# Optimization experiments

Hardware: AMD Instinct MI355X
Metric: run time of the kernel (lower is better)

Reference implementation:

```python
import jax, jax.numpy as jnp
import numpy as np

C_S, C_P, C_H, H, P_QK, P_V = 384, 128, 16, 12, 4, 8
B, N = 1, 512
INF = 1e5
EPS = 1e-8


def quat_to_rot(q):
    w, x, y, z = q[..., 0], q[..., 1], q[..., 2], q[..., 3]
    return jnp.stack([
        jnp.stack([1 - 2 * (y * y + z * z), 2 * (x * y - w * z), 2 * (x * z + w * y)], -1),
        jnp.stack([2 * (x * y + w * z), 1 - 2 * (x * x + z * z), 2 * (y * z - w * x)], -1),
        jnp.stack([2 * (x * z - w * y), 2 * (y * z + w * x), 1 - 2 * (x * x + y * y)], -1),
    ], -2)


def layer_norm(x, g, b):
    m = x.mean(-1, keepdims=True)
    v = ((x - m) ** 2).mean(-1, keepdims=True)
    return (x - m) * jax.lax.rsqrt(v + 1e-5) * g + b


def setup_inputs():
    key = jax.random.key(0)
    ks = iter(jax.random.split(key, 64))

    def w(shape, scale=0.02):
        return jax.random.normal(next(ks), shape, dtype=jnp.float32) * scale

    inp = {}
    inp['s'] = jax.random.normal(next(ks), (B, N, C_S), dtype=jnp.float32)
    inp['p'] = jax.random.normal(next(ks), (B, N, N, C_P), dtype=jnp.float32)
    q = jax.random.normal(next(ks), (B, N, 4), dtype=jnp.float32)
    inp['rot'] = quat_to_rot(q / jnp.linalg.norm(q, axis=-1, keepdims=True))
    inp['trans'] = jax.random.normal(next(ks), (B, N, 3), dtype=jnp.float32)
    inp['mask'] = jnp.ones((B, N), dtype=jnp.float32)
    inp['w_q'] = w((C_S, H * C_H)); inp['b_q'] = jnp.zeros((H * C_H,), jnp.float32)
    inp['w_kv'] = w((C_S, 2 * H * C_H)); inp['b_kv'] = jnp.zeros((2 * H * C_H,), jnp.float32)
    inp['w_qp'] = w((C_S, H * P_QK * 3)); inp['b_qp'] = jnp.zeros((H * P_QK * 3,), jnp.float32)
    inp['w_kvp'] = w((C_S, H * (P_QK + P_V) * 3)); inp['b_kvp'] = jnp.zeros((H * (P_QK + P_V) * 3,), jnp.float32)
    inp['w_b'] = w((C_P, H)); inp['b_b'] = jnp.zeros((H,), jnp.float32)
    inp['head_w'] = w((H,), 0.5)
    d_out = H * (C_H + C_P + P_V * 4)  # 2112
    inp['w_o'] = w((d_out, C_S)); inp['b_o'] = jnp.zeros((C_S,), jnp.float32)
    inp['ln1_g'] = jnp.ones((C_S,), jnp.float32); inp['ln1_b'] = jnp.zeros((C_S,), jnp.float32)
    for i in (1, 2, 3):
        inp['tw%d' % i] = w((C_S, C_S)); inp['tb%d' % i] = jnp.zeros((C_S,), jnp.float32)
    inp['ln2_g'] = jnp.ones((C_S,), jnp.float32); inp['ln2_b'] = jnp.zeros((C_S,), jnp.float32)
    inp['bb_w'] = w((C_S, 6)); inp['bb_b'] = jnp.zeros((6,), jnp.float32)
    return inp


def forward(s, p, rot, trans, mask, w_q, b_q, w_kv, b_kv, w_qp, b_qp, w_kvp, b_kvp,
            w_b, b_b, head_w, w_o, b_o, ln1_g, ln1_b,
            tw1, tb1, tw2, tb2, tw3, tb3, ln2_g, ln2_b, bb_w, bb_b):
    # ---- Invariant Point Attention ----
    q = (s @ w_q + b_q).reshape(B, N, H, C_H)
    k, v = jnp.split((s @ w_kv + b_kv).reshape(B, N, H, 2 * C_H), 2, axis=-1)
    qp = (s @ w_qp + b_qp).reshape(B, N, H * P_QK, 3)
    qp = (jnp.einsum('bnij,bnpj->bnpi', rot, qp) + trans[:, :, None, :]).reshape(B, N, H, P_QK, 3)
    kvp = (s @ w_kvp + b_kvp).reshape(B, N, H * (P_QK + P_V), 3)
    kvp = (jnp.einsum('bnij,bnpj->bnpi', rot, kvp) + trans[:, :, None, :]).reshape(B, N, H, P_QK + P_V, 3)
    kp, vp = kvp[..., :P_QK, :], kvp[..., P_QK:, :]
    bias = p @ w_b + b_b  # [B,N,N,H]
    a = jnp.einsum('bihc,bjhc->bhij', q, k) * float(np.sqrt(1.0 / (3 * C_H)))
    a = a + float(np.sqrt(1.0 / 3)) * jnp.transpose(bias, (0, 3, 1, 2))
    d2 = ((qp[:, :, None] - kp[:, None]) ** 2).sum(-1)  # [B,N,N,H,Pqk]
    hw = jax.nn.softplus(head_w) * float(np.sqrt(1.0 / (3 * (P_QK * 9.0 / 2))))
    pt_att = -0.5 * (d2 * hw[:, None]).sum(-1)  # [B,N,N,H]
    sq_mask = (mask[:, :, None] * mask[:, None, :] - 1.0) * INF  # [B,N,N]
    a = jax.nn.softmax(a + jnp.transpose(pt_att, (0, 3, 1, 2)) + sq_mask[:, None], axis=-1)
    o = jnp.einsum('bhij,bjhc->bihc', a, v).reshape(B, N, H * C_H)
    op = jnp.einsum('bhij,bjhpc->bihpc', a, vp) - trans[:, :, None, None, :]
    op = jnp.einsum('bnji,bnhpj->bnhpi', rot, op)  # invert-apply frames
    op_norm = jnp.sqrt((op ** 2).sum(-1) + EPS)  # [B,N,H,Pv]
    o_pair = jnp.einsum('bhij,bijc->bihc', a, p).reshape(B, N, H * C_P)
    cat = jnp.concatenate([o, op.reshape(B, N, H * P_V * 3), op_norm.reshape(B, N, H * P_V), o_pair], -1)
    s = s + cat @ w_o + b_o
    s = layer_norm(s, ln1_g, ln1_b)
    # ---- structure transition (1 layer, residual + LN) ----
    h = jax.nn.relu(s @ tw1 + tb1)
    h = jax.nn.relu(h @ tw2 + tb2)
    s = layer_norm(s + h @ tw3 + tb3, ln2_g, ln2_b)
    # ---- backbone update + frame compose ----
    upd = s @ bb_w + bb_b  # [B,N,6]
    quat = jnp.concatenate([jnp.ones((B, N, 1), s.dtype), upd[..., :3]], -1)
    quat = quat / jnp.linalg.norm(quat, axis=-1, keepdims=True)
    r_u = quat_to_rot(quat)
    rot_new = jnp.einsum('bnij,bnjk->bnik', rot, r_u)
    trans_new = jnp.einsum('bnij,bnj->bni', rot, upd[..., 3:]) + trans
    return s, rot_new, trans_new


def reference(s, p, rot, trans, mask, w_q, b_q, w_kv, b_kv, w_qp, b_qp, w_kvp, b_kvp,
              w_b, b_b, head_w, w_o, b_o, ln1_g, ln1_b,
              tw1, tb1, tw2, tb2, tw3, tb3, ln2_g, ln2_b, bb_w, bb_b):
    return forward(s, p, rot, trans, mask, w_q, b_q, w_kv, b_kv, w_qp, b_qp, w_kvp, b_kvp,
                   w_b, b_b, head_w, w_o, b_o, ln1_g, ln1_b,
                   tw1, tb1, tw2, tb2, tw3, tb3, ln2_g, ln2_b, bb_w, bb_b)
```

## Files before the change

kernel.cpp:

```cpp
#include <hip/hip_runtime.h>
#include <math.h>

#define N 512
#define CS 384
#define CP 128
#define CH 16
#define NH 12
#define NN (N*N)
#define DCAT 2112
#define INFV 100000.0f

__device__ __constant__ float SC_QK = 0.14433756729740643f;
#define SC_B  0.57735026918962576f
#define HW_SC 0.13608276348795434f

typedef __attribute__((ext_vector_type(8))) short bf16x8;
typedef __attribute__((ext_vector_type(4))) float f32x4;
typedef __attribute__((ext_vector_type(4))) short sh4;
typedef unsigned short ushort_t;

__device__ inline short f2bf(float v) {
    unsigned u = __builtin_bit_cast(unsigned, v);
    u += 0x7FFF + ((u >> 16) & 1);
    return (short)(u >> 16);
}
__device__ inline float bf2f(ushort_t u) {
    unsigned x = ((unsigned)u) << 16;
    return __builtin_bit_cast(float, x);
}
__device__ __forceinline__ unsigned cvtpk(float a, float b) {
    unsigned r;
    asm("v_cvt_pk_bf16_f32 %0, %1, %2" : "=v"(r) : "v"(a), "v"(b));
    return r;
}

__device__ __forceinline__ void gload16(const void* g, void* l) {
    __builtin_amdgcn_global_load_lds(
        (const __attribute__((address_space(1))) unsigned int*)g,
        (__attribute__((address_space(3))) unsigned int*)l,
        16, 0, 0);
}

struct PrepArgs {
    const float* wsrc0; const float* wsrc1; const float* wsrc2; const float* wsrc3;
    const float* wsrc4; const float* wsrc5; const float* wsrc6; const float* wsrc7;
    ushort_t* wdst0; ushort_t* wdst1; ushort_t* wdst2; ushort_t* wdst3;
    ushort_t* wdst4; ushort_t* wdst5; ushort_t* wdst6; ushort_t* wdst7;
    const float* s; ushort_t* sbf;
    const float* bq; const float* bkv; const float* bqp; const float* bkvp;
    float* biasp;
};

__global__ __launch_bounds__(256) void prep_kernel(PrepArgs a)
{
    const int b = blockIdx.x;
    if (b < 1668) {
        const float* src; ushort_t* dst; int begin, nx, Nc, K;
        if      (b < 72)   { src=a.wsrc0; dst=a.wdst0; begin=0;    nx=6;  Nc=192; K=384; }
        else if (b < 216)  { src=a.wsrc1; dst=a.wdst1; begin=72;   nx=12; Nc=384; K=384; }
        else if (b < 276)  { src=a.wsrc2; dst=a.wdst2; begin=216;  nx=5;  Nc=144; K=384; }
        else if (b < 444)  { src=a.wsrc3; dst=a.wdst3; begin=276;  nx=14; Nc=432; K=384; }
        else if (b < 1236) { src=a.wsrc4; dst=a.wdst4; begin=444;  nx=12; Nc=384; K=2112; }
        else if (b < 1380) { src=a.wsrc5; dst=a.wdst5; begin=1236; nx=12; Nc=384; K=384; }
        else if (b < 1524) { src=a.wsrc6; dst=a.wdst6; begin=1380; nx=12; Nc=384; K=384; }
        else               { src=a.wsrc7; dst=a.wdst7; begin=1524; nx=12; Nc=384; K=384; }
        int lb = b - begin;
        int cx = (lb % nx) * 32, ky = (lb / nx) * 32;
        __shared__ float tile[32][33];
        const int tx = threadIdx.x & 31, ty = threadIdx.x >> 5;
        for (int r = ty; r < 32; r += 8) {
            int c = cx + tx;
            tile[r][tx] = (c < Nc) ? src[(size_t)(ky + r) * Nc + c] : 0.f;
        }
        __syncthreads();
        for (int r = ty; r < 32; r += 8) {
            int orow = cx + r;
            if (orow < Nc)
                dst[(size_t)orow * K + ky + tx] = (ushort_t)f2bf(tile[tx][r]);
        }
    } else if (b < 1860) {
        int i4 = (b - 1668) * 256 + threadIdx.x;
        f32x4 v = *(const f32x4*)(a.s + (size_t)i4 * 4);
        sh4 o;
        o[0] = f2bf(v[0]); o[1] = f2bf(v[1]); o[2] = f2bf(v[2]); o[3] = f2bf(v[3]);
        *(sh4*)(a.sbf + (size_t)i4 * 4) = o;
    } else {
        for (int idx = threadIdx.x; idx < 1152; idx += 256) {
            float v;
            if (idx < 192)      v = a.bq[idx];
            else if (idx < 576) v = a.bkv[idx - 192];
            else if (idx < 720) v = a.bqp[idx - 576];
            else                v = a.bkvp[idx - 720];
            a.biasp[idx] = v;
        }
    }
}

__global__ __launch_bounds__(256) void gemm_bf16(
    const ushort_t* __restrict__ A, const ushort_t* __restrict__ Bt,
    float* __restrict__ part, int K, int KOUT, int nk)
{
    __shared__ __align__(16) ushort_t As[2][2048];
    __shared__ __align__(16) ushort_t Bs[2][2048];
    const int t = threadIdx.x, w = t >> 6, l = t & 63;
    const int i0 = blockIdx.x * 64, n0 = blockIdx.y * 64, sp = blockIdx.z;
    const int kbase = sp * nk * 32;

    const int srow = w * 16 + (l >> 2);
    const int skb = (l & 3) ^ ((srow >> 1) & 3);
    const ushort_t* aSrc = A + (size_t)(i0 + srow) * K + kbase + skb * 8;
    const ushort_t* bSrc = Bt + (size_t)(n0 + srow) * K + kbase + skb * 8;
    ushort_t* aDst = &As[0][0] + w * 512;
    ushort_t* bDst = &Bs[0][0] + w * 512;

    const int r0 = (w >> 1) * 32, c0 = (w & 1) * 32, lr = l & 15, hk = l >> 4;
    int aOff[2], bOff[2];
    #pragma unroll
    for (int m = 0; m < 2; ++m) {
        int row = r0 + m * 16 + lr;
        aOff[m] = row * 64 + ((hk ^ ((row >> 1) & 3)) << 4);
    }
    #pragma unroll
    for (int n = 0; n < 2; ++n) {
        int row = c0 + n * 16 + lr;
        bOff[n] = row * 64 + ((hk ^ ((row >> 1) & 3)) << 4);
    }

    f32x4 acc[2][2];
    #pragma unroll
    for (int m = 0; m < 2; ++m)
        #pragma unroll
        for (int n = 0; n < 2; ++n) acc[m][n] = (f32x4){0.f, 0.f, 0.f, 0.f};

    gload16(aSrc, aDst);
    gload16(bSrc, bDst);
    __syncthreads();

    int cur = 0;
    for (int it = 0; it < nk; ++it) {
        if (it + 1 < nk) {
            gload16(aSrc + (it + 1) * 32, aDst + (cur ^ 1) * 2048);
            gload16(bSrc + (it + 1) * 32, bDst + (cur ^ 1) * 2048);
        }
        const char* ab = (const char*)&As[cur][0];
        const char* bb = (const char*)&Bs[cur][0];
        bf16x8 a0 = *(const bf16x8*)(ab + aOff[0]);
        bf16x8 a1 = *(const bf16x8*)(ab + aOff[1]);
        bf16x8 b0 = *(const bf16x8*)(bb + bOff[0]);
        bf16x8 b1 = *(const bf16x8*)(bb + bOff[1]);
        acc[0][0] = __builtin_amdgcn_mfma_f32_16x16x32_bf16(a0, b0, acc[0][0], 0, 0, 0);
        acc[0][1] = __builtin_amdgcn_mfma_f32_16x16x32_bf16(a0, b1, acc[0][1], 0, 0, 0);
        acc[1][0] = __builtin_amdgcn_mfma_f32_16x16x32_bf16(a1, b0, acc[1][0], 0, 0, 0);
        acc[1][1] = __builtin_amdgcn_mfma_f32_16x16x32_bf16(a1, b1, acc[1][1], 0, 0, 0);
        __syncthreads();
        cur ^= 1;
    }

    #pragma unroll
    for (int m = 0; m < 2; ++m)
        #pragma unroll
        for (int n = 0; n < 2; ++n) {
            int col = n0 + c0 + n * 16 + lr;
            int rowb = i0 + r0 + m * 16 + (l >> 4) * 4;
            float* pr = part + ((size_t)sp * 512 + rowb) * KOUT + col;
            #pragma unroll
            for (int j = 0; j < 4; ++j)
                pr[(size_t)j * KOUT] = acc[m][n][j];
        }
}

__global__ void reduce_k(const float* __restrict__ parts, int S, int KOUT,
                         const float* __restrict__ bias, const float* __restrict__ resid,
                         int relu, float* __restrict__ outf, ushort_t* __restrict__ outbf)
{
    int i4 = blockIdx.x * 256 + threadIdx.x;
    int tot = 512 * KOUT / 4;
    if (i4 >= tot) return;
    int idx = i4 * 4, c = idx % KOUT;
    f32x4 v = *(const f32x4*)(bias + c);
    for (int s2 = 0; s2 < S; ++s2)
        v += *(const f32x4*)(parts + (size_t)s2 * 512 * KOUT + idx);
    if (resid) v += *(const f32x4*)(resid + idx);
    if (relu) {
        v[0] = fmaxf(v[0], 0.f); v[1] = fmaxf(v[1], 0.f);
        v[2] = fmaxf(v[2], 0.f); v[3] = fmaxf(v[3], 0.f);
    }
    if (outf) *(f32x4*)(outf + idx) = v;
    if (outbf) {
        sh4 o;
        o[0] = f2bf(v[0]); o[1] = f2bf(v[1]); o[2] = f2bf(v[2]); o[3] = f2bf(v[3]);
        *(sh4*)(outbf + idx) = o;
    }
}

__global__ void reduce_ln(const float* __restrict__ parts, int S,
                          const float* __restrict__ gbias, const float* __restrict__ resid,
                          const float* __restrict__ g, const float* __restrict__ b,
                          float* __restrict__ outf, ushort_t* __restrict__ outbf,
                          const float* __restrict__ bb_w, const float* __restrict__ bb_b,
                          const float* __restrict__ rot, const float* __restrict__ trans,
                          float* __restrict__ out_rot, float* __restrict__ out_trans)
{
    __shared__ float buf[384];
    __shared__ float red[2], red2[2];
    __shared__ float ush[2][6];
    const int i = blockIdx.x, t = threadIdx.x;
    float s = 0.f, sq = 0.f;
    for (int k = t; k < 384; k += 128) {
        float v = gbias[k] + resid[(size_t)i * 384 + k];
        for (int s2 = 0; s2 < S; ++s2)
            v += parts[((size_t)s2 * 512 + i) * 384 + k];
        buf[k] = v; s += v; sq += v * v;
    }
    for (int off = 32; off; off >>= 1) { s += __shfl_xor(s, off); sq += __shfl_xor(sq, off); }
    if ((t & 63) == 0) { red[t >> 6] = s; red2[t >> 6] = sq; }
    __syncthreads();
    float mean = (red[0] + red[1]) * (1.0f / 384.0f);
    float var = (red2[0] + red2[1]) * (1.0f / 384.0f) - mean * mean;
    float rstd = rsqrtf(var + 1e-5f);
    float onorm[3];
    #pragma unroll
    for (int kk = 0; kk < 3; ++kk) {
        int k = t + kk * 128;
        float o = (buf[k] - mean) * rstd * g[k] + b[k];
        onorm[kk] = o;
        if (outf) outf[(size_t)i * 384 + k] = o;
        if (outbf) outbf[(size_t)i * 384 + k] = (ushort_t)f2bf(o);
    }
    if (!bb_w) return;
    float u[6] = {0.f, 0.f, 0.f, 0.f, 0.f, 0.f};
    #pragma unroll
    for (int kk = 0; kk < 3; ++kk) {
        int k = t + kk * 128;
        float sv = onorm[kk];
        #pragma unroll
        for (int c = 0; c < 6; ++c) u[c] += sv * bb_w[k * 6 + c];
    }
    #pragma unroll
    for (int c = 0; c < 6; ++c)
        for (int off = 32; off; off >>= 1) u[c] += __shfl_xor(u[c], off);
    if ((t & 63) == 0) {
        #pragma unroll
        for (int c = 0; c < 6; ++c) ush[t >> 6][c] = u[c];
    }
    __syncthreads();
    if (t == 0) {
        float uu[6];
        #pragma unroll
        for (int c = 0; c < 6; ++c) uu[c] = ush[0][c] + ush[1][c] + bb_b[c];
        float inq = rsqrtf(1.0f + uu[0]*uu[0] + uu[1]*uu[1] + uu[2]*uu[2]);
        float w = inq, x = uu[0]*inq, y = uu[1]*inq, z = uu[2]*inq;
        float Ru[9];
        Ru[0] = 1.f - 2.f*(y*y + z*z); Ru[1] = 2.f*(x*y - w*z); Ru[2] = 2.f*(x*z + w*y);
        Ru[3] = 2.f*(x*y + w*z); Ru[4] = 1.f - 2.f*(x*x + z*z); Ru[5] = 2.f*(y*z - w*x);
        Ru[6] = 2.f*(x*z - w*y); Ru[7] = 2.f*(y*z + w*x); Ru[8] = 1.f - 2.f*(x*x + y*y);
        const float* R = rot + i * 9;
        #pragma unroll
        for (int a = 0; a < 3; ++a) {
            #pragma unroll
            for (int cc = 0; cc < 3; ++cc)
                out_rot[i * 9 + a * 3 + cc] =
                    R[a*3+0]*Ru[0+cc] + R[a*3+1]*Ru[3+cc] + R[a*3+2]*Ru[6+cc];
            out_trans[i * 3 + a] = R[a*3+0]*uu[3] + R[a*3+1]*uu[4] + R[a*3+2]*uu[5]
                                   + trans[i * 3 + a];
        }
    }
}

__global__ __launch_bounds__(256) void postproj_kernel(
    const float* __restrict__ parts, const float* __restrict__ biasp,
    const float* __restrict__ rot, const float* __restrict__ trans,
    const float* __restrict__ head_w, const float* __restrict__ mask,
    ushort_t* __restrict__ Qext, ushort_t* __restrict__ Kext, ushort_t* __restrict__ Vext)
{
    __shared__ float buf[1152];
    __shared__ float hwv[12], kc28[12];
    const int j = blockIdx.x, t = threadIdx.x;
    for (int c = t; c < 1152; c += 256)
        buf[c] = biasp[c] + parts[(size_t)j * 1152 + c] + parts[(size_t)(512 + j) * 1152 + c];
    if (t >= 192 && t < 204) {
        int h = t - 192;
        hwv[h] = HW_SC * log1pf(expf(head_w[h]));
    }
    __syncthreads();
    if (t < 192) {
        int base = 576 + t * 3;
        const float* R = rot + j * 9;
        const float* T = trans + j * 3;
        float x = buf[base], y = buf[base + 1], z = buf[base + 2];
        float nx = R[0]*x + R[1]*y + R[2]*z + T[0];
        float ny = R[3]*x + R[4]*y + R[5]*z + T[1];
        float nz = R[6]*x + R[7]*y + R[8]*z + T[2];
        buf[base] = nx; buf[base + 1] = ny; buf[base + 2] = nz;
    }
    __syncthreads();
    if (t < 12) {
        float s2 = 0.f;
        #pragma unroll
        for (int e = 0; e < 12; ++e) { float v = buf[720 + t * 36 + e]; s2 += v * v; }
        kc28[t] = -0.5f * hwv[t] * s2 + (mask[j] - 1.0f) * INFV;
    }
    __syncthreads();
    if (t < 192) {
        int h = t >> 4, c0 = (t & 15) * 2;
        float hwf = hwv[h];
        #pragma unroll
        for (int e = 0; e < 2; ++e) {
            int c = c0 + e;
            float qv, kv2;
            if (c < 16)      { qv = SC_QK * buf[h * 16 + c];           kv2 = buf[192 + h * 32 + c]; }
            else if (c < 28) { qv = hwf * buf[576 + h * 12 + (c - 16)]; kv2 = buf[720 + h * 36 + (c - 16)]; }
            else if (c == 28){ qv = 1.f;                               kv2 = kc28[h]; }
            else             { qv = 0.f;                               kv2 = 0.f; }
            Qext[(size_t)h * 16384 + j * 32 + c] = (ushort_t)f2bf(qv);
            Kext[(size_t)h * 16384 + j * 32 + c] = (ushort_t)f2bf(kv2);
        }
    }
    for (int idx = t; idx < 576; idx += 256) {
        int h = idx / 48, c = idx % 48;
        float v;
        if (c < 16)      v = buf[192 + h * 32 + 16 + c];
        else if (c < 40) v = buf[720 + h * 36 + 12 + (c - 16)];
        else             v = 0.f;
        Vext[(size_t)h * 24576 + c * 512 + j] = (ushort_t)f2bf(v);
    }
}

__global__ __launch_bounds__(256) void bias_mfma(
    const float* __restrict__ p, const float* __restrict__ w_b,
    const float* __restrict__ b_b, ushort_t* __restrict__ bias_b)
{
    __shared__ __align__(16) float Pf[64 * 128];
    __shared__ __align__(16) ushort_t Wbs[16 * 128];
    const int t = threadIdx.x, w = t >> 6;
    const size_t row0 = (size_t)blockIdx.x * 64;

    for (int idx = t; idx < 2048; idx += 256) {
        int h = idx >> 7, c = idx & 127;
        float v = (h < 12) ? w_b[c * 12 + h] : 0.f;
        int byte = h * 256 + ((c * 2) ^ ((h & 7) << 4));
        *(ushort_t*)((char*)Wbs + byte) = (ushort_t)f2bf(v);
    }
    #pragma unroll
    for (int k = 0; k < 8; ++k) {
        int s = k * 256 + t;
        int row = s >> 5, ch = s & 31;
        const char* src = (const char*)(p + (row0 + row) * 128) + ((ch ^ (row & 7)) * 16);
        gload16(src, (char*)Pf + (size_t)(k * 256 + w * 64) * 16);
    }
    __syncthreads();

    const int l = t & 63, lr = l & 15, hk = l >> 4;
    const int jb = w * 16;
    f32x4 acc = (f32x4){0.f, 0.f, 0.f, 0.f};
    #pragma unroll
    for (int ks = 0; ks < 4; ++ks) {
        int row = jb + lr;
        int kc = ks * 8 + hk * 2;
        const char* base = (const char*)Pf + row * 512;
        f32x4 v0 = *(const f32x4*)(base + ((kc ^ (row & 7)) * 16));
        f32x4 v1 = *(const f32x4*)(base + (((kc + 1) ^ (row & 7)) * 16));
        bf16x8 afr;
        afr[0] = f2bf(v0[0]); afr[1] = f2bf(v0[1]); afr[2] = f2bf(v0[2]); afr[3] = f2bf(v0[3]);
        afr[4] = f2bf(v1[0]); afr[5] = f2bf(v1[1]); afr[6] = f2bf(v1[2]); afr[7] = f2bf(v1[3]);
        bf16x8 bfr = *(const bf16x8*)((char*)Wbs + lr * 256 +
                        ((ks * 64 + hk * 16) ^ ((lr & 7) << 4)));
        acc = __builtin_amdgcn_mfma_f32_16x16x32_bf16(afr, bfr, acc, 0, 0, 0);
    }
    if (lr < 12) {
        float bb = b_b[lr];
        size_t gj = row0 + jb + hk * 4;
        sh4 o;
        #pragma unroll
        for (int r = 0; r < 4; ++r) o[r] = f2bf(SC_B * (acc[r] + bb));
        *(sh4*)(bias_b + (size_t)lr * NN + gj) = o;
    }
}

__global__ __launch_bounds__(256) void attn_mfma(
    const ushort_t* __restrict__ Qext, const ushort_t* __restrict__ Kext,
    const ushort_t* __restrict__ bias_b, ushort_t* __restrict__ attn_b)
{
    __shared__ float sc[32 * 516];
    __shared__ float redm[128];
    __shared__ float invr[32];
    const int t = threadIdx.x, w = t >> 6, l = t & 63;
    const int i0 = blockIdx.x * 32, h = blockIdx.y;
    const int lr = l & 15, hk = l >> 4;

    #pragma unroll
    for (int it = 0; it < 16; ++it) {
        int elem = (t + it * 256) * 4;
        int i = elem >> 9, j = elem & 511;
        sh4 raw = *(const sh4*)(bias_b + (size_t)h * NN + (size_t)(i0 + i) * 512 + j);
        f32x4 v;
        v[0] = bf2f((ushort_t)raw[0]); v[1] = bf2f((ushort_t)raw[1]);
        v[2] = bf2f((ushort_t)raw[2]); v[3] = bf2f((ushort_t)raw[3]);
        *(f32x4*)(sc + i * 516 + j) = v;
    }
    __syncthreads();

    bf16x8 a0 = *(const bf16x8*)(Qext + (size_t)h * 16384 + (i0 + lr) * 32 + hk * 8);
    bf16x8 a1 = *(const bf16x8*)(Qext + (size_t)h * 16384 + (i0 + 16 + lr) * 32 + hk * 8);
    f32x4 acc[2][8];
    #pragma unroll
    for (int n = 0; n < 8; ++n) {
        bf16x8 b = *(const bf16x8*)(Kext + (size_t)h * 16384 +
                                    (w * 128 + n * 16 + lr) * 32 + hk * 8);
        acc[0][n] = __builtin_amdgcn_mfma_f32_16x16x32_bf16(a0, b, (f32x4){0.f,0.f,0.f,0.f}, 0, 0, 0);
        acc[1][n] = __builtin_amdgcn_mfma_f32_16x16x32_bf16(a1, b, (f32x4){0.f,0.f,0.f,0.f}, 0, 0, 0);
    }

    float rmax[2][4];
    #pragma unroll
    for (int m = 0; m < 2; ++m)
        #pragma unroll
        for (int r = 0; r < 4; ++r) rmax[m][r] = -3.0e38f;
    #pragma unroll
    for (int m = 0; m < 2; ++m)
        #pragma unroll
        for (int n = 0; n < 8; ++n) {
            int col = w * 128 + n * 16 + lr;
            #pragma unroll
            for (int r = 0; r < 4; ++r) {
                int row = m * 16 + hk * 4 + r;
                float v = acc[m][n][r] + sc[row * 516 + col];
                sc[row * 516 + col] = v;
                rmax[m][r] = fmaxf(rmax[m][r], v);
            }
        }
    #pragma unroll
    for (int m = 0; m < 2; ++m)
        #pragma unroll
        for (int r = 0; r < 4; ++r) {
            float v = rmax[m][r];
            v = fmaxf(v, __shfl_xor(v, 1));
            v = fmaxf(v, __shfl_xor(v, 2));
            v = fmaxf(v, __shfl_xor(v, 4));
            v = fmaxf(v, __shfl_xor(v, 8));
            if (lr == 0) redm[w * 32 + m * 16 + hk * 4 + r] = v;
        }
    __syncthreads();

    {
        int row = t >> 3, g = t & 7;
        float mx = fmaxf(fmaxf(redm[row], redm[32 + row]),
                         fmaxf(redm[64 + row], redm[96 + row]));
        float sum = 0.f;
        float* sr = sc + row * 516;
        for (int c = g; c < 512; c += 8) {
            float e = expf(sr[c] - mx);
            sr[c] = e;
            sum += e;
        }
        sum += __shfl_xor(sum, 1);
        sum += __shfl_xor(sum, 2);
        sum += __shfl_xor(sum, 4);
        if (g == 0) invr[row] = 1.0f / sum;
    }
    __syncthreads();

    #pragma unroll
    for (int it = 0; it < 16; ++it) {
        int elem = (t + it * 256) * 4;
        int i = elem >> 9, j = elem & 511;
        f32x4 v = *(const f32x4*)(sc + i * 516 + j);
        float iv = invr[i];
        sh4 o;
        o[0] = f2bf(v[0] * iv); o[1] = f2bf(v[1] * iv);
        o[2] = f2bf(v[2] * iv); o[3] = f2bf(v[3] * iv);
        *(sh4*)(attn_b + (size_t)h * NN + (size_t)(i0 + i) * 512 + j) = o;
    }
}

__global__ __launch_bounds__(64) void ov_mfma(
    const ushort_t* __restrict__ attn_b, const ushort_t* __restrict__ Vext,
    const float* __restrict__ rot, const float* __restrict__ trans,
    ushort_t* __restrict__ catb)
{
    __shared__ float opl[16][25];
    const int l = threadIdx.x;
    const int i0 = blockIdx.x * 16, h = blockIdx.y;
    const int lr = l & 15, hk = l >> 4;
    f32x4 acc[3];
    acc[0] = (f32x4){0.f,0.f,0.f,0.f};
    acc[1] = (f32x4){0.f,0.f,0.f,0.f};
    acc[2] = (f32x4){0.f,0.f,0.f,0.f};
    const ushort_t* arow = attn_b + (size_t)h * NN + (size_t)(i0 + lr) * 512 + hk * 8;
    const ushort_t* vbase = Vext + (size_t)h * 24576 + lr * 512 + hk * 8;
    #pragma unroll
    for (int kt = 0; kt < 16; ++kt) {
        bf16x8 af = *(const bf16x8*)(arow + kt * 32);
        #pragma unroll
        for (int n = 0; n < 3; ++n) {
            bf16x8 bf = *(const bf16x8*)(vbase + n * 16 * 512 + kt * 32);
            acc[n] = __builtin_amdgcn_mfma_f32_16x16x32_bf16(af, bf, acc[n], 0, 0, 0);
        }
    }
    #pragma unroll
    for (int n = 0; n < 3; ++n) {
        int c = n * 16 + lr;
        #pragma unroll
        for (int r = 0; r < 4; ++r) {
            int ri = hk * 4 + r;
            if (c < 16)
                catb[(size_t)(i0 + ri) * DCAT + h * 16 + c] = (ushort_t)f2bf(acc[n][r]);
            else if (c < 40)
                opl[ri][c - 16] = acc[n][r];
        }
    }
    __syncthreads();
    #pragma unroll
    for (int e = 0; e < 2; ++e) {
        int pt = l + e * 64;
        int i16 = pt >> 3, pv = pt & 7;
        int i = i0 + i16;
        const float* T = trans + i * 3;
        const float* R = rot + i * 9;
        float x = opl[i16][pv * 3 + 0] - T[0];
        float y = opl[i16][pv * 3 + 1] - T[1];
        float z = opl[i16][pv * 3 + 2] - T[2];
        float rx = R[0] * x + R[3] * y + R[6] * z;
        float ry = R[1] * x + R[4] * y + R[7] * z;
        float rz = R[2] * x + R[5] * y + R[8] * z;
        float nm = sqrtf(rx * rx + ry * ry + rz * rz + 1e-8f);
        ushort_t* cr = catb + (size_t)i * DCAT;
        cr[192 + h * 24 + pv * 3 + 0] = (ushort_t)f2bf(rx);
        cr[192 + h * 24 + pv * 3 + 1] = (ushort_t)f2bf(ry);
        cr[192 + h * 24 + pv * 3 + 2] = (ushort_t)f2bf(rz);
        cr[480 + h * 8 + pv] = (ushort_t)f2bf(nm);
    }
}

__global__ __launch_bounds__(256) void opair_mfma(
    const ushort_t* __restrict__ attn_b, const float* __restrict__ p,
    ushort_t* __restrict__ catb)
{
    __shared__ __align__(16) ushort_t As2[16 * 512];
    __shared__ __align__(16) ushort_t Pt[2][128 * 72];
    const int t = threadIdx.x, i = blockIdx.x;
    const int w = t >> 6, l = t & 63;
    const int lr = l & 15, hk = l >> 4;

    #pragma unroll
    for (int ii = 0; ii < 4; ++ii) {
        int idx = (t + ii * 256) * 8;
        int h = idx >> 9, j = idx & 511;
        bf16x8 v;
        if (h < 12) v = *(const bf16x8*)(attn_b + (size_t)h * NN + (size_t)i * 512 + j);
        else        v = (bf16x8){0,0,0,0,0,0,0,0};
        *(bf16x8*)((char*)As2 + h * 1024 + ((j * 2) ^ ((h & 7) << 4))) = v;
    }

    const int jA = (t >> 3) * 2;
    const int c0 = (t & 7) * 16;
    const float* psrc = p + (size_t)i * 65536;

    f32x4 va[4], vb[4];
    #pragma unroll
    for (int q = 0; q < 4; ++q) {
        va[q] = *(const f32x4*)(psrc + (size_t)jA * 128 + c0 + q * 4);
        vb[q] = *(const f32x4*)(psrc + (size_t)(jA + 1) * 128 + c0 + q * 4);
    }

    #define PACK_TILE(buf)                                                       \
        {                                                                        \
            ushort_t* ptw = &Pt[buf][0];                                         \
            _Pragma("unroll")                                                    \
            for (int e = 0; e < 16; ++e) {                                       \
                int c = c0 + e;                                                  \
                unsigned pk = cvtpk(va[e >> 2][e & 3], vb[e >> 2][e & 3]);       \
                int byte = c * 144 + ((jA * 2) ^ (((c >> 4) & 7) << 4));         \
                *(unsigned*)((char*)ptw + byte) = pk;                            \
            }                                                                    \
        }
    #define LOAD_TILE(tile)                                                      \
        {                                                                        \
            const float* s0 = psrc + (size_t)((tile) * 64 + jA) * 128 + c0;      \
            _Pragma("unroll")                                                    \
            for (int q = 0; q < 4; ++q) {                                        \
                va[q] = *(const f32x4*)(s0 + q * 4);                             \
                vb[q] = *(const f32x4*)(s0 + 128 + q * 4);                       \
            }                                                                    \
        }

    PACK_TILE(0);
    LOAD_TILE(1);

    f32x4 acc[2];
    acc[0] = (f32x4){0.f, 0.f, 0.f, 0.f};
    acc[1] = (f32x4){0.f, 0.f, 0.f, 0.f};

    int cur = 0;
    for (int tile = 0; tile < 8; ++tile) {
        __syncthreads();
        const char* pt = (const char*)&Pt[cur][0];
        #pragma unroll
        for (int ks = 0; ks < 2; ++ks) {
            bf16x8 afr = *(const bf16x8*)((char*)As2 + lr * 1024 +
                            ((tile * 128 + ks * 64 + hk * 16) ^ ((lr & 7) << 4)));
            #pragma unroll
            for (int n = 0; n < 2; ++n) {
                int c = w * 32 + n * 16 + lr;
                bf16x8 bfr = *(const bf16x8*)(pt + c * 144 +
                                ((ks * 64 + hk * 16) ^ (((c >> 4) & 7) << 4)));
                acc[n] = __builtin_amdgcn_mfma_f32_16x16x32_bf16(afr, bfr, acc[n], 0, 0, 0);
            }
        }
        if (tile < 7) {
            PACK_TILE(cur ^ 1);
            if (tile < 6) LOAD_TILE(tile + 2);
            cur ^= 1;
        }
    }
    #undef PACK_TILE
    #undef LOAD_TILE
    #pragma unroll
    for (int n = 0; n < 2; ++n) {
        int c = w * 32 + n * 16 + lr;
        #pragma unroll
        for (int r = 0; r < 4; ++r) {
            int h = hk * 4 + r;
            if (h < 12)
                catb[(size_t)i * DCAT + 576 + h * 128 + c] = (ushort_t)f2bf(acc[n][r]);
        }
    }
}

extern "C" void kernel_launch(void* const* d_in, const int* in_sizes, int n_in,
                              void* d_out, int out_size, void* d_ws, size_t ws_size,
                              hipStream_t stream)
{
    const float* s      = (const float*)d_in[0];
    const float* p      = (const float*)d_in[1];
    const float* rot    = (const float*)d_in[2];
    const float* trans  = (const float*)d_in[3];
    const float* mask   = (const float*)d_in[4];
    const float* w_q    = (const float*)d_in[5];
    const float* b_q    = (const float*)d_in[6];
    const float* w_kv   = (const float*)d_in[7];
    const float* b_kv   = (const float*)d_in[8];
    const float* w_qp   = (const float*)d_in[9];
    const float* b_qp   = (const float*)d_in[10];
    const float* w_kvp  = (const float*)d_in[11];
    const float* b_kvp  = (const float*)d_in[12];
    const float* w_b    = (const float*)d_in[13];
    const float* b_b    = (const float*)d_in[14];
    const float* head_w = (const float*)d_in[15];
    const float* w_o    = (const float*)d_in[16];
    const float* b_o    = (const float*)d_in[17];
    const float* ln1_g  = (const float*)d_in[18];
    const float* ln1_b  = (const float*)d_in[19];
    const float* tw1    = (const float*)d_in[20];
    const float* tb1    = (const float*)d_in[21];
    const float* tw2    = (const float*)d_in[22];
    const float* tb2    = (const float*)d_in[23];
    const float* tw3    = (const float*)d_in[24];
    const float* tb3    = (const float*)d_in[25];
    const float* ln2_g  = (const float*)d_in[26];
    const float* ln2_b  = (const float*)d_in[27];
    const float* bb_w   = (const float*)d_in[28];
    const float* bb_b   = (const float*)d_in[29];

    float* ws = (float*)d_ws;
    float*    parts = ws;
    float*    s1    = parts + 1179648;
    float*    biasp = s1 + 196608;
    ushort_t* ub     = (ushort_t*)(biasp + 1152);
    ushort_t* bias_b = ub;
    ushort_t* attn_b = bias_b + 3145728;
    ushort_t* catb   = attn_b + 3145728;
    ushort_t* sbf    = catb + 1081344;
    ushort_t* s1bf   = sbf + 196608;
    ushort_t* h1bf   = s1bf + 196608;
    ushort_t* h2bf   = h1bf + 196608;
    ushort_t* Qext   = h2bf + 196608;
    ushort_t* Kext   = Qext + 196608;
    ushort_t* Vext   = Kext + 196608;
    ushort_t* Wtp    = Vext + 294912;
    ushort_t* Wto    = Wtp + 442368;
    ushort_t* Wt1    = Wto + 811008;
    ushort_t* Wt2    = Wt1 + 147456;
    ushort_t* Wt3    = Wt2 + 147456;

    float* out_s     = (float*)d_out;
    float* out_rot   = out_s + 196608;
    float* out_trans = out_rot + 4608;

    PrepArgs pa;
    pa.wsrc0 = w_q;  pa.wdst0 = Wtp;
    pa.wsrc1 = w_kv; pa.wdst1 = Wtp + (size_t)192 * 384;
    pa.wsrc2 = w_qp; pa.wdst2 = Wtp + (size_t)576 * 384;
    pa.wsrc3 = w_kvp; pa.wdst3 = Wtp + (size_t)720 * 384;
    pa.wsrc4 = w_o;  pa.wdst4 = Wto;
    pa.wsrc5 = tw1;  pa.wdst5 = Wt1;
    pa.wsrc6 = tw2;  pa.wdst6 = Wt2;
    pa.wsrc7 = tw3;  pa.wdst7 = Wt3;
    pa.s = s; pa.sbf = sbf;
    pa.bq = b_q; pa.bkv = b_kv; pa.bqp = b_qp; pa.bkvp = b_kvp;
    pa.biasp = biasp;
    prep_kernel<<<1861, 256, 0, stream>>>(pa);

    gemm_bf16<<<dim3(8, 18, 2), 256, 0, stream>>>(sbf, Wtp, parts, 384, 1152, 6);
    postproj_kernel<<<512, 256, 0, stream>>>(parts, biasp, rot, trans, head_w, mask,
                                             Qext, Kext, Vext);

    bias_mfma<<<4096, 256, 0, stream>>>(p, w_b, b_b, bias_b);
    attn_mfma<<<dim3(16, 12), 256, 0, stream>>>(Qext, Kext, bias_b, attn_b);
    ov_mfma<<<dim3(32, 12), 64, 0, stream>>>(attn_b, Vext, rot, trans, catb);
    opair_mfma<<<512, 256, 0, stream>>>(attn_b, p, catb);

    gemm_bf16<<<dim3(8, 6, 6), 256, 0, stream>>>(catb, Wto, parts, 2112, 384, 11);
    reduce_ln<<<512, 128, 0, stream>>>(parts, 6, b_o, s, ln1_g, ln1_b, s1, s1bf,
                                       nullptr, nullptr, nullptr, nullptr, nullptr, nullptr);

    gemm_bf16<<<dim3(8, 6, 3), 256, 0, stream>>>(s1bf, Wt1, parts, 384, 384, 4);
    reduce_k<<<192, 256, 0, stream>>>(parts, 3, 384, tb1, nullptr, 1, nullptr, h1bf);
    gemm_bf16<<<dim3(8, 6, 3), 256, 0, stream>>>(h1bf, Wt2, parts, 384, 384, 4);
    reduce_k<<<192, 256, 0, stream>>>(parts, 3, 384, tb2, nullptr, 1, nullptr, h2bf);
    gemm_bf16<<<dim3(8, 6, 3), 256, 0, stream>>>(h2bf, Wt3, parts, 384, 384, 4);
    reduce_ln<<<512, 128, 0, stream>>>(parts, 3, tb3, s1, ln2_g, ln2_b, out_s, nullptr,
                                       bb_w, bb_b, rot, trans, out_rot, out_trans);
}
```

Before: 130.0 us.

## Fuse attn with OV product and merge tail into one cooperative kernel

The attention kernel now handles 16 query rows per block and computes the attention-times-V product straight from the softmax scores in shared memory, scaling by the inverse row sum at the end. This removes the separate ov kernel and its reread of attn_b. The tail of the network (output projection, layer norm, three transition GEMMs with reductions, final LN and frame update) becomes one cooperative kernel of 256 blocks, with grid syncs between phases and a fixed 5-way K split. This cuts about ten kernel launches, at the cost of grid-sync overhead and fewer blocks for the large output GEMM.

```diff
diff --git a/kernel.cpp b/kernel.cpp
--- a/kernel.cpp
+++ b/kernel.cpp
@@ -1,5 +1,8 @@
 #include <hip/hip_runtime.h>
+#include <hip/hip_cooperative_groups.h>
 #include <math.h>
+
+namespace cg = cooperative_groups;
 
 #define N 512
 #define CS 384
@@ -17,6 +20,7 @@
 typedef __attribute__((ext_vector_type(8))) short bf16x8;
 typedef __attribute__((ext_vector_type(4))) float f32x4;
 typedef __attribute__((ext_vector_type(4))) short sh4;
+typedef __attribute__((ext_vector_type(4))) unsigned u32x4;
 typedef unsigned short ushort_t;
 
 __device__ inline short f2bf(float v) {
@@ -169,104 +173,6 @@
         }
 }
 
-__global__ void reduce_k(const float* __restrict__ parts, int S, int KOUT,
-                         const float* __restrict__ bias, const float* __restrict__ resid,
-                         int relu, float* __restrict__ outf, ushort_t* __restrict__ outbf)
-{
-    int i4 = blockIdx.x * 256 + threadIdx.x;
-    int tot = 512 * KOUT / 4;
-    if (i4 >= tot) return;
-    int idx = i4 * 4, c = idx % KOUT;
-    f32x4 v = *(const f32x4*)(bias + c);
-    for (int s2 = 0; s2 < S; ++s2)
-        v += *(const f32x4*)(parts + (size_t)s2 * 512 * KOUT + idx);
-    if (resid) v += *(const f32x4*)(resid + idx);
-    if (relu) {
-        v[0] = fmaxf(v[0], 0.f); v[1] = fmaxf(v[1], 0.f);
-        v[2] = fmaxf(v[2], 0.f); v[3] = fmaxf(v[3], 0.f);
-    }
-    if (outf) *(f32x4*)(outf + idx) = v;
-    if (outbf) {
-        sh4 o;
-        o[0] = f2bf(v[0]); o[1] = f2bf(v[1]); o[2] = f2bf(v[2]); o[3] = f2bf(v[3]);
-        *(sh4*)(outbf + idx) = o;
-    }
-}
-
-__global__ void reduce_ln(const float* __restrict__ parts, int S,
-                          const float* __restrict__ gbias, const float* __restrict__ resid,
-                          const float* __restrict__ g, const float* __restrict__ b,
-                          float* __restrict__ outf, ushort_t* __restrict__ outbf,
-                          const float* __restrict__ bb_w, const float* __restrict__ bb_b,
-                          const float* __restrict__ rot, const float* __restrict__ trans,
-                          float* __restrict__ out_rot, float* __restrict__ out_trans)
-{
-    __shared__ float buf[384];
-    __shared__ float red[2], red2[2];
-    __shared__ float ush[2][6];
-    const int i = blockIdx.x, t = threadIdx.x;
-    float s = 0.f, sq = 0.f;
-    for (int k = t; k < 384; k += 128) {
-        float v = gbias[k] + resid[(size_t)i * 384 + k];
-        for (int s2 = 0; s2 < S; ++s2)
-            v += parts[((size_t)s2 * 512 + i) * 384 + k];
-        buf[k] = v; s += v; sq += v * v;
-    }
-    for (int off = 32; off; off >>= 1) { s += __shfl_xor(s, off); sq += __shfl_xor(sq, off); }
-    if ((t & 63) == 0) { red[t >> 6] = s; red2[t >> 6] = sq; }
-    __syncthreads();
-    float mean = (red[0] + red[1]) * (1.0f / 384.0f);
-    float var = (red2[0] + red2[1]) * (1.0f / 384.0f) - mean * mean;
-    float rstd = rsqrtf(var + 1e-5f);
-    float onorm[3];
-    #pragma unroll
-    for (int kk = 0; kk < 3; ++kk) {
-        int k = t + kk * 128;
-        float o = (buf[k] - mean) * rstd * g[k] + b[k];
-        onorm[kk] = o;
-        if (outf) outf[(size_t)i * 384 + k] = o;
-        if (outbf) outbf[(size_t)i * 384 + k] = (ushort_t)f2bf(o);
-    }
-    if (!bb_w) return;
-    float u[6] = {0.f, 0.f, 0.f, 0.f, 0.f, 0.f};
-    #pragma unroll
-    for (int kk = 0; kk < 3; ++kk) {
-        int k = t + kk * 128;
-        float sv = onorm[kk];
-        #pragma unroll
-        for (int c = 0; c < 6; ++c) u[c] += sv * bb_w[k * 6 + c];
-    }
-    #pragma unroll
-    for (int c = 0; c < 6; ++c)
-        for (int off = 32; off; off >>= 1) u[c] += __shfl_xor(u[c], off);
-    if ((t & 63) == 0) {
-        #pragma unroll
-        for (int c = 0; c < 6; ++c) ush[t >> 6][c] = u[c];
-    }
-    __syncthreads();
-    if (t == 0) {
-        float uu[6];
-        #pragma unroll
-        for (int c = 0; c < 6; ++c) uu[c] = ush[0][c] + ush[1][c] + bb_b[c];
-        float inq = rsqrtf(1.0f + uu[0]*uu[0] + uu[1]*uu[1] + uu[2]*uu[2]);
-        float w = inq, x = uu[0]*inq, y = uu[1]*inq, z = uu[2]*inq;
-        float Ru[9];
-        Ru[0] = 1.f - 2.f*(y*y + z*z); Ru[1] = 2.f*(x*y - w*z); Ru[2] = 2.f*(x*z + w*y);
-        Ru[3] = 2.f*(x*y + w*z); Ru[4] = 1.f - 2.f*(x*x + z*z); Ru[5] = 2.f*(y*z - w*x);
-        Ru[6] = 2.f*(x*z - w*y); Ru[7] = 2.f*(y*z + w*x); Ru[8] = 1.f - 2.f*(x*x + y*y);
-        const float* R = rot + i * 9;
-        #pragma unroll
-        for (int a = 0; a < 3; ++a) {
-            #pragma unroll
-            for (int cc = 0; cc < 3; ++cc)
-                out_rot[i * 9 + a * 3 + cc] =
-                    R[a*3+0]*Ru[0+cc] + R[a*3+1]*Ru[3+cc] + R[a*3+2]*Ru[6+cc];
-            out_trans[i * 3 + a] = R[a*3+0]*uu[3] + R[a*3+1]*uu[4] + R[a*3+2]*uu[5]
-                                   + trans[i * 3 + a];
-        }
-    }
-}
-
 __global__ __launch_bounds__(256) void postproj_kernel(
     const float* __restrict__ parts, const float* __restrict__ biasp,
     const float* __restrict__ rot, const float* __restrict__ trans,
@@ -379,17 +285,20 @@
 
 __global__ __launch_bounds__(256) void attn_mfma(
     const ushort_t* __restrict__ Qext, const ushort_t* __restrict__ Kext,
-    const ushort_t* __restrict__ bias_b, ushort_t* __restrict__ attn_b)
-{
-    __shared__ float sc[32 * 516];
-    __shared__ float redm[128];
-    __shared__ float invr[32];
+    const ushort_t* __restrict__ bias_b, const ushort_t* __restrict__ Vext,
+    const float* __restrict__ rot, const float* __restrict__ trans,
+    ushort_t* __restrict__ attn_b, ushort_t* __restrict__ catb)
+{
+    __shared__ float sc[16 * 516];
+    __shared__ float redm[64];
+    __shared__ float invr[16];
+    __shared__ float opl[16][25];
     const int t = threadIdx.x, w = t >> 6, l = t & 63;
-    const int i0 = blockIdx.x * 32, h = blockIdx.y;
+    const int i0 = blockIdx.x * 16, h = blockIdx.y;
     const int lr = l & 15, hk = l >> 4;
 
     #pragma unroll
-    for (int it = 0; it < 16; ++it) {
+    for (int it = 0; it < 8; ++it) {
         int elem = (t + it * 256) * 4;
         int i = elem >> 9, j = elem & 511;
         sh4 raw = *(const sh4*)(bias_b + (size_t)h * NN + (size_t)(i0 + i) * 512 + j);
@@ -401,54 +310,44 @@
     __syncthreads();
 
     bf16x8 a0 = *(const bf16x8*)(Qext + (size_t)h * 16384 + (i0 + lr) * 32 + hk * 8);
-    bf16x8 a1 = *(const bf16x8*)(Qext + (size_t)h * 16384 + (i0 + 16 + lr) * 32 + hk * 8);
-    f32x4 acc[2][8];
+    f32x4 acc[8];
     #pragma unroll
     for (int n = 0; n < 8; ++n) {
         bf16x8 b = *(const bf16x8*)(Kext + (size_t)h * 16384 +
                                     (w * 128 + n * 16 + lr) * 32 + hk * 8);
-        acc[0][n] = __builtin_amdgcn_mfma_f32_16x16x32_bf16(a0, b, (f32x4){0.f,0.f,0.f,0.f}, 0, 0, 0);
-        acc[1][n] = __builtin_amdgcn_mfma_f32_16x16x32_bf16(a1, b, (f32x4){0.f,0.f,0.f,0.f}, 0, 0, 0);
-    }
-
-    float rmax[2][4];
-    #pragma unroll
-    for (int m = 0; m < 2; ++m)
-        #pragma unroll
-        for (int r = 0; r < 4; ++r) rmax[m][r] = -3.0e38f;
-    #pragma unroll
-    for (int m = 0; m < 2; ++m)
-        #pragma unroll
-        for (int n = 0; n < 8; ++n) {
-            int col = w * 128 + n * 16 + lr;
-            #pragma unroll
-            for (int r = 0; r < 4; ++r) {
-                int row = m * 16 + hk * 4 + r;
-                float v = acc[m][n][r] + sc[row * 516 + col];
-                sc[row * 516 + col] = v;
-                rmax[m][r] = fmaxf(rmax[m][r], v);
-            }
-        }
-    #pragma unroll
-    for (int m = 0; m < 2; ++m)
+        acc[n] = __builtin_amdgcn_mfma_f32_16x16x32_bf16(a0, b, (f32x4){0.f,0.f,0.f,0.f}, 0, 0, 0);
+    }
+
+    float rmax[4] = {-3.0e38f, -3.0e38f, -3.0e38f, -3.0e38f};
+    #pragma unroll
+    for (int n = 0; n < 8; ++n) {
+        int col = w * 128 + n * 16 + lr;
         #pragma unroll
         for (int r = 0; r < 4; ++r) {
-            float v = rmax[m][r];
-            v = fmaxf(v, __shfl_xor(v, 1));
-            v = fmaxf(v, __shfl_xor(v, 2));
-            v = fmaxf(v, __shfl_xor(v, 4));
-            v = fmaxf(v, __shfl_xor(v, 8));
-            if (lr == 0) redm[w * 32 + m * 16 + hk * 4 + r] = v;
-        }
+            int row = hk * 4 + r;
+            float v = acc[n][r] + sc[row * 516 + col];
+            sc[row * 516 + col] = v;
+            rmax[r] = fmaxf(rmax[r], v);
+        }
+    }
+    #pragma unroll
+    for (int r = 0; r < 4; ++r) {
+        float v = rmax[r];
+        v = fmaxf(v, __shfl_xor(v, 1));
+        v = fmaxf(v, __shfl_xor(v, 2));
+        v = fmaxf(v, __shfl_xor(v, 4));
+        v = fmaxf(v, __shfl_xor(v, 8));
+        if (lr == 0) redm[w * 16 + hk * 4 + r] = v;
+    }
     __syncthreads();
 
     {
-        int row = t >> 3, g = t & 7;
-        float mx = fmaxf(fmaxf(redm[row], redm[32 + row]),
-                         fmaxf(redm[64 + row], redm[96 + row]));
+        int row = t >> 4, g = t & 15;
+        float mx = fmaxf(fmaxf(redm[row], redm[16 + row]),
+                         fmaxf(redm[32 + row], redm[48 + row]));
         float sum = 0.f;
         float* sr = sc + row * 516;
-        for (int c = g; c < 512; c += 8) {
+        for (int c = g; c < 512; c += 16) {
             float e = expf(sr[c] - mx);
             sr[c] = e;
             sum += e;
@@ -456,12 +355,13 @@
         sum += __shfl_xor(sum, 1);
         sum += __shfl_xor(sum, 2);
         sum += __shfl_xor(sum, 4);
+        sum += __shfl_xor(sum, 8);
         if (g == 0) invr[row] = 1.0f / sum;
     }
     __syncthreads();
 
     #pragma unroll
-    for (int it = 0; it < 16; ++it) {
+    for (int it = 0; it < 8; ++it) {
         int elem = (t + it * 256) * 4;
         int i = elem >> 9, j = elem & 511;
         f32x4 v = *(const f32x4*)(sc + i * 516 + j);
@@ -471,30 +371,25 @@
         o[2] = f2bf(v[2] * iv); o[3] = f2bf(v[3] * iv);
         *(sh4*)(attn_b + (size_t)h * NN + (size_t)(i0 + i) * 512 + j) = o;
     }
-}
-
-__global__ __launch_bounds__(64) void ov_mfma(
-    const ushort_t* __restrict__ attn_b, const ushort_t* __restrict__ Vext,
-    const float* __restrict__ rot, const float* __restrict__ trans,
-    ushort_t* __restrict__ catb)
-{
-    __shared__ float opl[16][25];
-    const int l = threadIdx.x;
-    const int i0 = blockIdx.x * 16, h = blockIdx.y;
-    const int lr = l & 15, hk = l >> 4;
-    f32x4 acc[3];
-    acc[0] = (f32x4){0.f,0.f,0.f,0.f};
-    acc[1] = (f32x4){0.f,0.f,0.f,0.f};
-    acc[2] = (f32x4){0.f,0.f,0.f,0.f};
-    const ushort_t* arow = attn_b + (size_t)h * NN + (size_t)(i0 + lr) * 512 + hk * 8;
+
+    f32x4 acc3[3];
+    acc3[0] = (f32x4){0.f,0.f,0.f,0.f};
+    acc3[1] = (f32x4){0.f,0.f,0.f,0.f};
+    acc3[2] = (f32x4){0.f,0.f,0.f,0.f};
     const ushort_t* vbase = Vext + (size_t)h * 24576 + lr * 512 + hk * 8;
     #pragma unroll
     for (int kt = 0; kt < 16; ++kt) {
-        bf16x8 af = *(const bf16x8*)(arow + kt * 32);
+        const float* srow = sc + lr * 516 + kt * 32 + hk * 8;
+        f32x4 x0 = *(const f32x4*)(srow);
+        f32x4 x1 = *(const f32x4*)(srow + 4);
+        u32x4 ap;
+        ap[0] = cvtpk(x0[0], x0[1]); ap[1] = cvtpk(x0[2], x0[3]);
+        ap[2] = cvtpk(x1[0], x1[1]); ap[3] = cvtpk(x1[2], x1[3]);
+        bf16x8 af = __builtin_bit_cast(bf16x8, ap);
         #pragma unroll
         for (int n = 0; n < 3; ++n) {
             bf16x8 bf = *(const bf16x8*)(vbase + n * 16 * 512 + kt * 32);
-            acc[n] = __builtin_amdgcn_mfma_f32_16x16x32_bf16(af, bf, acc[n], 0, 0, 0);
+            acc3[n] = __builtin_amdgcn_mfma_f32_16x16x32_bf16(af, bf, acc3[n], 0, 0, 0);
         }
     }
     #pragma unroll
@@ -503,17 +398,16 @@
         #pragma unroll
         for (int r = 0; r < 4; ++r) {
             int ri = hk * 4 + r;
+            float val = acc3[n][r] * invr[ri];
             if (c < 16)
-                catb[(size_t)(i0 + ri) * DCAT + h * 16 + c] = (ushort_t)f2bf(acc[n][r]);
+                catb[(size_t)(i0 + ri) * DCAT + h * 16 + c] = (ushort_t)f2bf(val);
             else if (c < 40)
-                opl[ri][c - 16] = acc[n][r];
-        }
-    }
-    __syncthreads();
-    #pragma unroll
-    for (int e = 0; e < 2; ++e) {
-        int pt = l + e * 64;
-        int i16 = pt >> 3, pv = pt & 7;
+                opl[ri][c - 16] = val;
+        }
+    }
+    __syncthreads();
+    if (t < 128) {
+        int i16 = t >> 3, pv = t & 7;
         int i = i0 + i16;
         const float* T = trans + i * 3;
         const float* R = rot + i * 9;
@@ -625,6 +519,219 @@
                 catb[(size_t)i * DCAT + 576 + h * 128 + c] = (ushort_t)f2bf(acc[n][r]);
         }
     }
+}
+
+struct TailArgs {
+    const ushort_t* catb; const ushort_t* Wto; const float* b_o; const float* s;
+    float* parts; float* s1; ushort_t* s1bf;
+    const float* ln1_g; const float* ln1_b;
+    const ushort_t* Wt1; const float* tb1; ushort_t* h1bf;
+    const ushort_t* Wt2; const float* tb2; ushort_t* h2bf;
+    const ushort_t* Wt3; const float* tb3;
+    const float* ln2_g; const float* ln2_b;
+    float* out_s;
+    const float* bb_w; const float* bb_b; const float* rot; const float* trans;
+    float* out_rot; float* out_trans;
+};
+
+__device__ void gemm_phase(const ushort_t* A, const ushort_t* Bt, float* part,
+                           int K, int NKSTEPS)
+{
+    __shared__ __align__(16) ushort_t As[2][2048];
+    __shared__ __align__(16) ushort_t Bs[2][2048];
+    const int b = blockIdx.x;
+    if (b >= 240) return;
+    const int sp = b / 48, tile = b - sp * 48;
+    const int ib = tile / 6, nb = tile - (tile / 6) * 6;
+    const int kstart = (sp * NKSTEPS) / 5, kend = ((sp + 1) * NKSTEPS) / 5;
+    const int nk = kend - kstart;
+    const int kbase = kstart * 32;
+
+    const int t = threadIdx.x, w = t >> 6, l = t & 63;
+    const int i0 = ib * 64, n0 = nb * 64;
+
+    const int srow = w * 16 + (l >> 2);
+    const int skb = (l & 3) ^ ((srow >> 1) & 3);
+    const ushort_t* aSrc = A + (size_t)(i0 + srow) * K + kbase + skb * 8;
+    const ushort_t* bSrc = Bt + (size_t)(n0 + srow) * K + kbase + skb * 8;
+    ushort_t* aDst = &As[0][0] + w * 512;
+    ushort_t* bDst = &Bs[0][0] + w * 512;
+
+    const int r0 = (w >> 1) * 32, c0 = (w & 1) * 32, lr = l & 15, hk = l >> 4;
+    int aOff[2], bOff[2];
+    #pragma unroll
+    for (int m = 0; m < 2; ++m) {
+        int row = r0 + m * 16 + lr;
+        aOff[m] = row * 64 + ((hk ^ ((row >> 1) & 3)) << 4);
+    }
+    #pragma unroll
+    for (int n = 0; n < 2; ++n) {
+        int row = c0 + n * 16 + lr;
+        bOff[n] = row * 64 + ((hk ^ ((row >> 1) & 3)) << 4);
+    }
+
+    f32x4 acc[2][2];
+    #pragma unroll
+    for (int m = 0; m < 2; ++m)
+        #pragma unroll
+        for (int n = 0; n < 2; ++n) acc[m][n] = (f32x4){0.f, 0.f, 0.f, 0.f};
+
+    gload16(aSrc, aDst);
+    gload16(bSrc, bDst);
+    __syncthreads();
+
+    int cur = 0;
+    for (int it = 0; it < nk; ++it) {
+        if (it + 1 < nk) {
+            gload16(aSrc + (it + 1) * 32, aDst + (cur ^ 1) * 2048);
+            gload16(bSrc + (it + 1) * 32, bDst + (cur ^ 1) * 2048);
+        }
+        const char* ab = (const char*)&As[cur][0];
+        const char* bb = (const char*)&Bs[cur][0];
+        bf16x8 a0 = *(const bf16x8*)(ab + aOff[0]);
+        bf16x8 a1 = *(const bf16x8*)(ab + aOff[1]);
+        bf16x8 b0 = *(const bf16x8*)(bb + bOff[0]);
+        bf16x8 b1 = *(const bf16x8*)(bb + bOff[1]);
+        acc[0][0] = __builtin_amdgcn_mfma_f32_16x16x32_bf16(a0, b0, acc[0][0], 0, 0, 0);
+        acc[0][1] = __builtin_amdgcn_mfma_f32_16x16x32_bf16(a0, b1, acc[0][1], 0, 0, 0);
+        acc[1][0] = __builtin_amdgcn_mfma_f32_16x16x32_bf16(a1, b0, acc[1][0], 0, 0, 0);
+        acc[1][1] = __builtin_amdgcn_mfma_f32_16x16x32_bf16(a1, b1, acc[1][1], 0, 0, 0);
+        __syncthreads();
+        cur ^= 1;
+    }
+
+    #pragma unroll
+    for (int m = 0; m < 2; ++m)
+        #pragma unroll
+        for (int n = 0; n < 2; ++n) {
+            int col = n0 + c0 + n * 16 + lr;
+            int rowb = i0 + r0 + m * 16 + (l >> 4) * 4;
+            float* pr = part + ((size_t)sp * 512 + rowb) * 384 + col;
+            #pragma unroll
+            for (int j = 0; j < 4; ++j)
+                pr[(size_t)j * 384] = acc[m][n][j];
+        }
+}
+
+__device__ void reduce_phase(const float* parts, const float* bias, ushort_t* outbf)
+{
+    for (int i4 = blockIdx.x * 256 + threadIdx.x; i4 < 49152; i4 += 256 * 256) {
+        int idx = i4 * 4, c = idx % 384;
+        f32x4 v = *(const f32x4*)(bias + c);
+        #pragma unroll
+        for (int s2 = 0; s2 < 5; ++s2)
+            v += *(const f32x4*)(parts + (size_t)s2 * 196608 + idx);
+        v[0] = fmaxf(v[0], 0.f); v[1] = fmaxf(v[1], 0.f);
+        v[2] = fmaxf(v[2], 0.f); v[3] = fmaxf(v[3], 0.f);
+        sh4 o;
+        o[0] = f2bf(v[0]); o[1] = f2bf(v[1]); o[2] = f2bf(v[2]); o[3] = f2bf(v[3]);
+        *(sh4*)(outbf + idx) = o;
+    }
+}
+
+__device__ void ln_phase(const float* parts, const float* gbias, const float* resid,
+                         const float* g, const float* b, float* outf, ushort_t* outbf,
+                         bool dorigid, const TailArgs& a)
+{
+    __shared__ float buf[384];
+    __shared__ float red[2], red2[2];
+    __shared__ float ush[2][6];
+    const int t = threadIdx.x;
+    for (int i = blockIdx.x; i < 512; i += 256) {
+        float onorm[3];
+        if (t < 128) {
+            float s = 0.f, sq = 0.f;
+            #pragma unroll
+            for (int kk = 0; kk < 3; ++kk) {
+                int k = t + kk * 128;
+                float v = gbias[k] + resid[(size_t)i * 384 + k];
+                #pragma unroll
+                for (int s2 = 0; s2 < 5; ++s2)
+                    v += parts[(size_t)s2 * 196608 + (size_t)i * 384 + k];
+                buf[k] = v; s += v; sq += v * v;
+            }
+            for (int off = 32; off; off >>= 1) {
+                s += __shfl_xor(s, off); sq += __shfl_xor(sq, off);
+            }
+            if ((t & 63) == 0) { red[t >> 6] = s; red2[t >> 6] = sq; }
+        }
+        __syncthreads();
+        float mean = (red[0] + red[1]) * (1.0f / 384.0f);
+        float var = (red2[0] + red2[1]) * (1.0f / 384.0f) - mean * mean;
+        float rstd = rsqrtf(var + 1e-5f);
+        if (t < 128) {
+            #pragma unroll
+            for (int kk = 0; kk < 3; ++kk) {
+                int k = t + kk * 128;
+                float o = (buf[k] - mean) * rstd * g[k] + b[k];
+                onorm[kk] = o;
+                if (outf) outf[(size_t)i * 384 + k] = o;
+                if (outbf) outbf[(size_t)i * 384 + k] = (ushort_t)f2bf(o);
+            }
+        }
+        if (dorigid) {
+            if (t < 128) {
+                float u[6] = {0.f, 0.f, 0.f, 0.f, 0.f, 0.f};
+                #pragma unroll
+                for (int kk = 0; kk < 3; ++kk) {
+                    int k = t + kk * 128;
+                    float sv = onorm[kk];
+                    #pragma unroll
+                    for (int c = 0; c < 6; ++c) u[c] += sv * a.bb_w[k * 6 + c];
+                }
+                #pragma unroll
+                for (int c = 0; c < 6; ++c)
+                    for (int off = 32; off; off >>= 1) u[c] += __shfl_xor(u[c], off);
+                if ((t & 63) == 0) {
+                    #pragma unroll
+                    for (int c = 0; c < 6; ++c) ush[t >> 6][c] = u[c];
+                }
+            }
+            __syncthreads();
+            if (t == 0) {
+                float uu[6];
+                #pragma unroll
+                for (int c = 0; c < 6; ++c) uu[c] = ush[0][c] + ush[1][c] + a.bb_b[c];
+                float inq = rsqrtf(1.0f + uu[0]*uu[0] + uu[1]*uu[1] + uu[2]*uu[2]);
+                float w = inq, x = uu[0]*inq, y = uu[1]*inq, z = uu[2]*inq;
+                float Ru[9];
+                Ru[0] = 1.f - 2.f*(y*y + z*z); Ru[1] = 2.f*(x*y - w*z); Ru[2] = 2.f*(x*z + w*y);
+                Ru[3] = 2.f*(x*y + w*z); Ru[4] = 1.f - 2.f*(x*x + z*z); Ru[5] = 2.f*(y*z - w*x);
+                Ru[6] = 2.f*(x*z - w*y); Ru[7] = 2.f*(y*z + w*x); Ru[8] = 1.f - 2.f*(x*x + y*y);
+                const float* R = a.rot + i * 9;
+                #pragma unroll
+                for (int aa = 0; aa < 3; ++aa) {
+                    #pragma unroll
+                    for (int cc = 0; cc < 3; ++cc)
+                        a.out_rot[i * 9 + aa * 3 + cc] =
+                            R[aa*3+0]*Ru[0+cc] + R[aa*3+1]*Ru[3+cc] + R[aa*3+2]*Ru[6+cc];
+                    a.out_trans[i * 3 + aa] = R[aa*3+0]*uu[3] + R[aa*3+1]*uu[4]
+                                              + R[aa*3+2]*uu[5] + a.trans[i * 3 + aa];
+                }
+            }
+        }
+        __syncthreads();
+    }
+}
+
+__global__ __launch_bounds__(256) void tail_kernel(TailArgs a)
+{
+    cg::grid_group grid = cg::this_grid();
+    gemm_phase(a.catb, a.Wto, a.parts, 2112, 66);
+    grid.sync();
+    ln_phase(a.parts, a.b_o, a.s, a.ln1_g, a.ln1_b, a.s1, a.s1bf, false, a);
+    grid.sync();
+    gemm_phase(a.s1bf, a.Wt1, a.parts, 384, 12);
+    grid.sync();
+    reduce_phase(a.parts, a.tb1, a.h1bf);
+    grid.sync();
+    gemm_phase(a.h1bf, a.Wt2, a.parts, 384, 12);
+    grid.sync();
+    reduce_phase(a.parts, a.tb2, a.h2bf);
+    grid.sync();
+    gemm_phase(a.h2bf, a.Wt3, a.parts, 384, 12);
+    grid.sync();
+    ln_phase(a.parts, a.tb3, a.s1, a.ln2_g, a.ln2_b, a.out_s, nullptr, true, a);
 }
 
 extern "C" void kernel_launch(void* const* d_in, const int* in_sizes, int n_in,
@@ -706,19 +813,21 @@
                                              Qext, Kext, Vext);
 
     bias_mfma<<<4096, 256, 0, stream>>>(p, w_b, b_b, bias_b);
-    attn_mfma<<<dim3(16, 12), 256, 0, stream>>>(Qext, Kext, bias_b, attn_b);
-    ov_mfma<<<dim3(32, 12), 64, 0, stream>>>(attn_b, Vext, rot, trans, catb);
+    attn_mfma<<<dim3(32, 12), 256, 0, stream>>>(Qext, Kext, bias_b, Vext, rot, trans,
+                                                attn_b, catb);
     opair_mfma<<<512, 256, 0, stream>>>(attn_b, p, catb);
 
-    gemm_bf16<<<dim3(8, 6, 6), 256, 0, stream>>>(catb, Wto, parts, 2112, 384, 11);
-    reduce_ln<<<512, 128, 0, stream>>>(parts, 6, b_o, s, ln1_g, ln1_b, s1, s1bf,
-                                       nullptr, nullptr, nullptr, nullptr, nullptr, nullptr);
-
-    gemm_bf16<<<dim3(8, 6, 3), 256, 0, stream>>>(s1bf, Wt1, parts, 384, 384, 4);
-    reduce_k<<<192, 256, 0, stream>>>(parts, 3, 384, tb1, nullptr, 1, nullptr, h1bf);
-    gemm_bf16<<<dim3(8, 6, 3), 256, 0, stream>>>(h1bf, Wt2, parts, 384, 384, 4);
-    reduce_k<<<192, 256, 0, stream>>>(parts, 3, 384, tb2, nullptr, 1, nullptr, h2bf);
-    gemm_bf16<<<dim3(8, 6, 3), 256, 0, stream>>>(h2bf, Wt3, parts, 384, 384, 4);
-    reduce_ln<<<512, 128, 0, stream>>>(parts, 3, tb3, s1, ln2_g, ln2_b, out_s, nullptr,
-                                       bb_w, bb_b, rot, trans, out_rot, out_trans);
-}
+    TailArgs ta;
+    ta.catb = catb; ta.Wto = Wto; ta.b_o = b_o; ta.s = s;
+    ta.parts = parts; ta.s1 = s1; ta.s1bf = s1bf;
+    ta.ln1_g = ln1_g; ta.ln1_b = ln1_b;
+    ta.Wt1 = Wt1; ta.tb1 = tb1; ta.h1bf = h1bf;
+    ta.Wt2 = Wt2; ta.tb2 = tb2; ta.h2bf = h2bf;
+    ta.Wt3 = Wt3; ta.tb3 = tb3;
+    ta.ln2_g = ln2_g; ta.ln2_b = ln2_b;
+    ta.out_s = out_s;
+    ta.bb_w = bb_w; ta.bb_b = bb_b; ta.rot = rot; ta.trans = trans;
+    ta.out_rot = out_rot; ta.out_trans = out_trans;
+    void* args[] = { &ta };
+    hipLaunchCooperativeKernel((void*)tail_kernel, dim3(256), dim3(256), args, 0, stream);
+}
```

Measured after the change: 352.9 us. +171.5%, slower.
